# Kernel optimization log

Measured on AMD Instinct MI355X. Metric: run time of the kernel, lower is better.

Reference implementation:

```python
import jax, jax.numpy as jnp
import numpy as np

K = 3        # prediction_steps
SKIP = 1     # skip_step (forward default)
NEG = 64     # opt.negative_samples
EPS = 1e-11  # ExpNLLLoss epsilon


def setup_inputs() -> dict:
    key = jax.random.key(0)
    ks = jax.random.split(key, 8)
    B, C, H, W = 64, 256, 14, 14
    z = jax.random.normal(ks[0], (B, C, H, W), jnp.float32)
    c = jax.random.normal(ks[1], (B, C, H, W), jnp.float32)
    Wk = jax.random.normal(ks[2], (K, C, C), jnp.float32) / np.sqrt(C).astype(np.float32)
    inp = {"z": z, "c": c, "Wk": Wk}
    for k in range(1, K + 1):
        Hp = H - (k + SKIP)
        rows = Hp * W * B
        inp[f"neg_idx_k{k}"] = jax.random.randint(ks[2 + k], (rows * NEG,), 0, rows, dtype=jnp.int32)
    return inp


def _loss_k(z, c, Wk, neg_idx, k):
    # z, c: [B,C,H,W]; Wk: [Co,Ci] (1x1 conv); neg_idx: [(H-k-SKIP)*W*B*NEG]
    B, C, H, W = z.shape
    Hp = H - (k + SKIP)
    zt = z[:, :, k + SKIP:, :]                            # [B,Ci,Hp,W]
    ztwk = jnp.einsum('oc,bchw->hwbo', Wk, zt)            # [Hp,W,B,Co] (1x1 conv + permute(2,3,0,1))
    flat = ztwk.reshape(Hp * W * B, -1)
    shuf = flat[neg_idx].reshape(Hp, W, B, NEG, -1)       # gathered negatives [Hp,W,B,N,Co]
    ctx = jnp.transpose(c[:, :, :Hp, :], (2, 3, 0, 1))    # context c[:,:,:-(k+SKIP),:] -> [Hp,W,B,Co]
    main = jnp.einsum('hwbc,hwbc->hwb', ctx, ztwk)[..., None]   # [Hp,W,B,1]
    negs = jnp.einsum('hwbc,hwbnc->hwbn', ctx, shuf)            # [Hp,W,B,N]
    log_fk = jnp.concatenate([main, negs], axis=-1)             # [Hp,W,B,1+N]
    log_fk = jnp.transpose(log_fk, (2, 3, 0, 1))                # [B,1+N,Hp,W]
    probs = jax.nn.softmax(log_fk, axis=1)
    # ExpNLLLoss, target class 0, reduction='mean'
    return -jnp.mean(jnp.log(probs[:, 0] + EPS))


def reference(z, c, Wk, neg_idx_k1, neg_idx_k2, neg_idx_k3):
    idxs = [neg_idx_k1, neg_idx_k2, neg_idx_k3]
    total = 0.0
    for k in range(1, K + 1):
        total = total + _loss_k(z, c, Wk[k - 1], idxs[k - 1], k)
    return total / K
```

## Files before the change

### kernel.cpp

```cpp
#include <hip/hip_runtime.h>
#include <math.h>


typedef short bf16x8 __attribute__((ext_vector_type(8)));
typedef float f32x4 __attribute__((ext_vector_type(4)));

static __device__ __forceinline__ unsigned short f2bf(float f) {
    union { float f; unsigned int u; } x; x.f = f;
    unsigned int r = x.u + 0x7fffu + ((x.u >> 16) & 1u);
    return (unsigned short)(r >> 16);
}

static __device__ __forceinline__ unsigned char f2e4m3(float f) {
    union { float f; unsigned int u; } x; x.f = f;
    unsigned int s = (x.u >> 24) & 0x80u;
    float af = fabsf(f);
    if (af > 448.f) af = 448.f;
    x.f = af;
    unsigned int u = x.u;
    int e = (int)(u >> 23) - 127;
    unsigned int out;
    if (af == 0.f) {
        out = 0u;
    } else if (e < -6) {
        int mq = (int)rintf(af * 512.f);
        out = (mq >= 8) ? 0x08u : (unsigned int)mq;
    } else {
        unsigned int r = u + 0x7FFFFu + ((u >> 20) & 1u);
        int e2 = (int)(r >> 23) - 127;
        if (e2 > 8) out = 0x7Eu;
        else out = (unsigned int)(((e2 + 7) << 3) | ((r >> 20) & 7u));
    }
    return (unsigned char)(s | out);
}

static __device__ __forceinline__ void gload_lds4(const void* g, void* l) {
    __builtin_amdgcn_global_load_lds(
        (const __attribute__((address_space(1))) void*)g,
        (__attribute__((address_space(3))) void*)l, 4, 0, 0);
}

__global__ __launch_bounds__(256)
void prep_kernel(const float* __restrict__ z, const float* __restrict__ c,
                 const float* __restrict__ Wk,
                 unsigned short* __restrict__ zt, unsigned char* __restrict__ ct8,
                 unsigned short* __restrict__ wkb, float* __restrict__ out) {
    __shared__ float tile[16][201];
    const int tid = threadIdx.x;
    int x = blockIdx.x;
    if (x < 768) {
        int i = x * 256 + tid;
        wkb[i] = f2bf(Wk[i]);
        if (x == 0 && tid == 0) out[0] = 0.f;
        return;
    }
    const bool isz = x < 1792;
    const int local = isz ? (x - 768) : (x - 1792);
    const float* src = isz ? z : c;
    const int b  = local & 63;
    const int c0 = (local >> 6) << 4;
    for (int i = tid; i < 16 * 196; i += 256) {
        int cc = i / 196;
        int hw = i - cc * 196;
        tile[cc][hw] = src[(size_t)((b << 8) + c0 + cc) * 196 + hw];
    }
    __syncthreads();
    if (isz) {
        for (int i = tid; i < 196 * 16; i += 256) {
            int hw = i >> 4, cc = i & 15;
            zt[(size_t)((hw << 6) + b) * 256 + c0 + cc] = f2bf(tile[cc][hw]);
        }
    } else {
        for (int i = tid; i < 196 * 16; i += 256) {
            int hw = i >> 4, cc = i & 15;
            ct8[(size_t)((hw << 6) + b) * 256 + c0 + cc] = f2e4m3(tile[cc][hw]);
        }
    }
}

#define PSTR 544
__global__ __launch_bounds__(256)
void proj_mfma_kernel(const unsigned short* __restrict__ zt,
                      const unsigned short* __restrict__ wkb,
                      unsigned char* __restrict__ ztwk) {
    __shared__ __align__(16) unsigned char smem[(64 + 32) * PSTR];
    unsigned char* smA = smem;
    unsigned char* smB = smem + 64 * PSTR;

    int x = blockIdx.x;
    int k, hw;
    if (x < 168)      { k = 0; hw = x; }
    else if (x < 322) { k = 1; hw = x - 168; }
    else              { k = 2; hw = x - 322; }
    const int o0 = blockIdx.y << 5;
    const int row0  = hw << 6;
    const int zrow0 = row0 + (((k + 2) * 14) << 6);
    unsigned char* zo = ztwk + (size_t)k * 10752 * 256;

    const int tid = threadIdx.x;
    const unsigned char* zsrc = (const unsigned char*)(zt + (size_t)zrow0 * 256);
    const unsigned char* bsrc = (const unsigned char*)(wkb + ((size_t)k << 16) + o0 * 256);

    #pragma unroll
    for (int i = 0; i < 8; ++i) {
        int sb = ((i << 8) + tid) << 4;
        int r = sb >> 9, off = sb & 511;
        *(int4*)(smA + r * PSTR + off) = *(const int4*)(zsrc + sb);
    }
    #pragma unroll
    for (int i = 0; i < 4; ++i) {
        int sb = ((i << 8) + tid) << 4;
        int r = sb >> 9, off = sb & 511;
        *(int4*)(smB + r * PSTR + off) = *(const int4*)(bsrc + sb);
    }
    __syncthreads();

    const int wv = tid >> 6, lane = tid & 63;
    const int m = lane & 15, kq = lane >> 4;
    f32x4 acc[2] = {};
    const unsigned short* aP  = (const unsigned short*)(smA + (size_t)((wv << 4) + m) * PSTR) + (kq << 3);
    const unsigned short* bP0 = (const unsigned short*)(smB + (size_t)m * PSTR) + (kq << 3);
    const unsigned short* bP1 = (const unsigned short*)(smB + (size_t)(16 + m) * PSTR) + (kq << 3);
    #pragma unroll
    for (int kk = 0; kk < 256; kk += 32) {
        bf16x8 af = *(const bf16x8*)(aP  + kk);
        bf16x8 b0 = *(const bf16x8*)(bP0 + kk);
        bf16x8 b1 = *(const bf16x8*)(bP1 + kk);
        acc[0] = __builtin_amdgcn_mfma_f32_16x16x32_bf16(af, b0, acc[0], 0, 0, 0);
        acc[1] = __builtin_amdgcn_mfma_f32_16x16x32_bf16(af, b1, acc[1], 0, 0, 0);
    }
    __syncthreads();
    unsigned char* cs = smA;
    #pragma unroll
    for (int nt = 0; nt < 2; ++nt)
        #pragma unroll
        for (int r = 0; r < 4; ++r)
            cs[(size_t)((wv << 4) + (kq << 2) + r) * 40 + (nt << 4) + m] =
                f2e4m3(acc[nt][r]);
    __syncthreads();
    {
        int r = tid >> 2, off = (tid & 3) << 3;
        unsigned long long v = *(const unsigned long long*)(cs + (size_t)r * 40 + off);
        *(unsigned long long*)(zo + (size_t)(row0 + r) * 256 + o0 + off) = v;
    }
}

#define ROWB 272
#define TPB 16
__global__ __launch_bounds__(128, 2)
void loss_mfma_kernel(const unsigned char* __restrict__ ct8,
                      const unsigned char* __restrict__ ztwk8,
                      const int* __restrict__ n0, const int* __restrict__ n1,
                      const int* __restrict__ n2, float* __restrict__ rowloss) {
    __shared__ __align__(16) unsigned char slab[2][65 * ROWB];
    __shared__ __align__(16) unsigned char ctx_s[2][256];
    const int tid = threadIdx.x;
    const int wv = tid >> 6, lane = tid & 63;
    const int m = lane & 15, kq = lane >> 4;

    const int task0 = blockIdx.x * TPB;
    int k; const int* nb; int segbase;
    if (task0 < 10752)      { k = 0; nb = n0; segbase = 0; }
    else if (task0 < 20608) { k = 1; nb = n1; segbase = 10752; }
    else                    { k = 2; nb = n2; segbase = 20608; }
    const int row0 = task0 - segbase;
    const unsigned char* flat8 = ztwk8 + (size_t)k * 10752 * 256;
    const float wkf = (k == 0) ? (1.f / (3.f * 10752.f))
                    : (k == 1) ? (1.f / (3.f * 9856.f))
                               : (1.f / (3.f * 8960.f));

    int myidx_next = 0;
    if (wv == 1) {
        int idx0 = nb[((size_t)row0 << 6) + lane];
        gload_lds4(flat8 + (size_t)row0 * 256 + (lane << 2), &slab[0][0]);
        gload_lds4(ct8 + (size_t)row0 * 256 + (lane << 2), &ctx_s[0][0]);
        #pragma unroll
        for (int j = 1; j <= 64; ++j) {
            int idx = __builtin_amdgcn_readlane(idx0, j - 1);
            gload_lds4(flat8 + (size_t)idx * 256 + (lane << 2), &slab[0][j * ROWB]);
        }
        myidx_next = nb[((size_t)(row0 + 1) << 6) + lane];
    }
    __syncthreads();

    int soff[5];
    #pragma unroll
    for (int mt = 0; mt < 5; ++mt) {
        int slot = (mt << 4) + m;
        if (slot > 64) slot = 64;
        soff[mt] = slot * ROWB + (kq << 3);
    }

    for (int t = 0; t < TPB; ++t) {
        const int buf = t & 1;
        if (wv == 1) {
            if (t + 1 < TPB) {
                const int rn = row0 + t + 1;
                const int nbuf = buf ^ 1;
                gload_lds4(flat8 + (size_t)rn * 256 + (lane << 2), &slab[nbuf][0]);
                gload_lds4(ct8 + (size_t)rn * 256 + (lane << 2), &ctx_s[nbuf][0]);
                #pragma unroll
                for (int j = 1; j <= 64; ++j) {
                    int idx = __builtin_amdgcn_readlane(myidx_next, j - 1);
                    gload_lds4(flat8 + (size_t)idx * 256 + (lane << 2),
                               &slab[nbuf][j * ROWB]);
                }
                if (t + 2 < TPB)
                    myidx_next = nb[((size_t)(row0 + t + 2) << 6) + lane];
            }
        } else {
            f32x4 acc[5] = {};
            const unsigned char* sl = &slab[buf][0];
            const unsigned char* cp = &ctx_s[buf][kq << 3];
            #pragma unroll
            for (int kk = 0; kk < 8; ++kk) {
                long long bfrag = *(const long long*)(cp + (kk << 5));
                #pragma unroll
                for (int mt = 0; mt < 5; ++mt) {
                    long long af = *(const long long*)(sl + soff[mt] + (kk << 5));
                    acc[mt] = __builtin_amdgcn_mfma_f32_16x16x32_fp8_fp8(
                        af, bfrag, acc[mt], 0, 0, 0);
                }
            }
            float m_l = -1e30f;
            #pragma unroll
            for (int mt = 0; mt < 4; ++mt)
                #pragma unroll
                for (int r = 0; r < 4; ++r) m_l = fmaxf(m_l, acc[mt][r]);
            if (kq == 0) m_l = fmaxf(m_l, acc[4][0]);
            m_l = fmaxf(m_l, __shfl_xor(m_l, 16));
            m_l = fmaxf(m_l, __shfl_xor(m_l, 32));
            float s_l = 0.f;
            #pragma unroll
            for (int mt = 0; mt < 4; ++mt)
                #pragma unroll
                for (int r = 0; r < 4; ++r) s_l += __expf(acc[mt][r] - m_l);
            if (kq == 0) s_l += __expf(acc[4][0] - m_l);
            s_l += __shfl_xor(s_l, 16);
            s_l += __shfl_xor(s_l, 32);
            if (lane == 0) {
                float p0 = __expf(acc[0][0] - m_l) / s_l;
                rowloss[segbase + row0 + t] = -logf(p0 + 1e-11f) * wkf;
            }
        }
        __syncthreads();
    }
}

__global__ __launch_bounds__(256)
void reduce_kernel(const float* __restrict__ rl, float* __restrict__ out) {
    float s = 0.f;
    const int stride = gridDim.x * blockDim.x;
    for (int i = blockIdx.x * blockDim.x + threadIdx.x; i < 29568; i += stride)
        s += rl[i];
    #pragma unroll
    for (int off = 32; off >= 1; off >>= 1) s += __shfl_xor(s, off);
    if ((threadIdx.x & 63) == 0) atomicAdd(out, s);
}

extern "C" void kernel_launch(void* const* d_in, const int* in_sizes, int n_in,
                              void* d_out, int out_size, void* d_ws, size_t ws_size,
                              hipStream_t stream) {
    const float* z  = (const float*)d_in[0];
    const float* c  = (const float*)d_in[1];
    const float* Wk = (const float*)d_in[2];
    const int* negs[3] = {(const int*)d_in[3], (const int*)d_in[4], (const int*)d_in[5]};
    float* out = (float*)d_out;

    char* p = (char*)d_ws;
    unsigned short* zt      = (unsigned short*)p;   p += (size_t)196 * 64 * 256 * 2;
    unsigned short* wkb     = (unsigned short*)p;   p += (size_t)3 * 65536 * 2;
    unsigned char*  ct8     = (unsigned char*)p;    p += (size_t)196 * 64 * 256;
    unsigned char*  ztwk8   = (unsigned char*)p;    p += (size_t)3 * 10752 * 256;
    float*          rowloss = (float*)p;

    prep_kernel<<<2816, 256, 0, stream>>>(z, c, Wk, zt, ct8, wkb, out);
    proj_mfma_kernel<<<dim3(462, 8), 256, 0, stream>>>(zt, wkb, ztwk8);
    loss_mfma_kernel<<<1848, 128, 0, stream>>>(ct8, ztwk8, negs[0], negs[1],
                                               negs[2], rowloss);
    reduce_kernel<<<32, 256, 0, stream>>>(rowloss, out);
}
```

Measured before the change: 167.8 us.

## Replace producer/consumer wave split with independent per-wave load-then-compute rows

```diff
diff --git a/kernel.cpp b/kernel.cpp
--- a/kernel.cpp
+++ b/kernel.cpp
@@ -146,43 +146,31 @@
 }
 
 #define ROWB 272
-#define TPB 16
-__global__ __launch_bounds__(128, 2)
+#define SLABSZ (65 * ROWB + 272)
+__global__ __launch_bounds__(128)
 void loss_mfma_kernel(const unsigned char* __restrict__ ct8,
                       const unsigned char* __restrict__ ztwk8,
                       const int* __restrict__ n0, const int* __restrict__ n1,
                       const int* __restrict__ n2, float* __restrict__ rowloss) {
-    __shared__ __align__(16) unsigned char slab[2][65 * ROWB];
-    __shared__ __align__(16) unsigned char ctx_s[2][256];
+    __shared__ __align__(16) unsigned char lds[2][SLABSZ];
     const int tid = threadIdx.x;
     const int wv = tid >> 6, lane = tid & 63;
     const int m = lane & 15, kq = lane >> 4;
-
-    const int task0 = blockIdx.x * TPB;
+    unsigned char* sl  = lds[wv];
+    unsigned char* ctx = sl + 65 * ROWB;
+
+    const int W = (blockIdx.x << 1) + wv;
+    const int base = W << 3;
     int k; const int* nb; int segbase;
-    if (task0 < 10752)      { k = 0; nb = n0; segbase = 0; }
-    else if (task0 < 20608) { k = 1; nb = n1; segbase = 10752; }
-    else                    { k = 2; nb = n2; segbase = 20608; }
-    const int row0 = task0 - segbase;
+    if (base < 10752)      { k = 0; nb = n0; segbase = 0; }
+    else if (base < 20608) { k = 1; nb = n1; segbase = 10752; }
+    else                   { k = 2; nb = n2; segbase = 20608; }
+    const int row0 = base - segbase;
     const unsigned char* flat8 = ztwk8 + (size_t)k * 10752 * 256;
     const float wkf = (k == 0) ? (1.f / (3.f * 10752.f))
                     : (k == 1) ? (1.f / (3.f * 9856.f))
                                : (1.f / (3.f * 8960.f));
 
-    int myidx_next = 0;
-    if (wv == 1) {
-        int idx0 = nb[((size_t)row0 << 6) + lane];
-        gload_lds4(flat8 + (size_t)row0 * 256 + (lane << 2), &slab[0][0]);
-        gload_lds4(ct8 + (size_t)row0 * 256 + (lane << 2), &ctx_s[0][0]);
-        #pragma unroll
-        for (int j = 1; j <= 64; ++j) {
-            int idx = __builtin_amdgcn_readlane(idx0, j - 1);
-            gload_lds4(flat8 + (size_t)idx * 256 + (lane << 2), &slab[0][j * ROWB]);
-        }
-        myidx_next = nb[((size_t)(row0 + 1) << 6) + lane];
-    }
-    __syncthreads();
-
     int soff[5];
     #pragma unroll
     for (int mt = 0; mt < 5; ++mt) {
@@ -191,59 +179,55 @@
         soff[mt] = slot * ROWB + (kq << 3);
     }
 
-    for (int t = 0; t < TPB; ++t) {
-        const int buf = t & 1;
-        if (wv == 1) {
-            if (t + 1 < TPB) {
-                const int rn = row0 + t + 1;
-                const int nbuf = buf ^ 1;
-                gload_lds4(flat8 + (size_t)rn * 256 + (lane << 2), &slab[nbuf][0]);
-                gload_lds4(ct8 + (size_t)rn * 256 + (lane << 2), &ctx_s[nbuf][0]);
-                #pragma unroll
-                for (int j = 1; j <= 64; ++j) {
-                    int idx = __builtin_amdgcn_readlane(myidx_next, j - 1);
-                    gload_lds4(flat8 + (size_t)idx * 256 + (lane << 2),
-                               &slab[nbuf][j * ROWB]);
-                }
-                if (t + 2 < TPB)
-                    myidx_next = nb[((size_t)(row0 + t + 2) << 6) + lane];
+    int myidx = nb[((size_t)row0 << 6) + lane];
+
+    for (int t = 0; t < 8; ++t) {
+        const int row = row0 + t;
+        asm volatile("s_waitcnt lgkmcnt(0)" ::: "memory");
+        gload_lds4(flat8 + (size_t)row * 256 + (lane << 2), sl);
+        gload_lds4(ct8 + (size_t)row * 256 + (lane << 2), ctx);
+        #pragma unroll
+        for (int j = 1; j <= 64; ++j) {
+            int idx = __builtin_amdgcn_readlane(myidx, j - 1);
+            gload_lds4(flat8 + (size_t)idx * 256 + (lane << 2), sl + j * ROWB);
+        }
+        asm volatile("s_waitcnt vmcnt(0)" ::: "memory");
+        if (t + 1 < 8)
+            myidx = nb[((size_t)(row + 1) << 6) + lane];
+
+        f32x4 acc[5] = {};
+        const unsigned char* cp = ctx + (kq << 3);
+        #pragma unroll
+        for (int kk = 0; kk < 8; ++kk) {
+            long long bfrag = *(const long long*)(cp + (kk << 5));
+            #pragma unroll
+            for (int mt = 0; mt < 5; ++mt) {
+                long long af = *(const long long*)(sl + soff[mt] + (kk << 5));
+                acc[mt] = __builtin_amdgcn_mfma_f32_16x16x32_fp8_fp8(
+                    af, bfrag, acc[mt], 0, 0, 0);
             }
-        } else {
-            f32x4 acc[5] = {};
-            const unsigned char* sl = &slab[buf][0];
-            const unsigned char* cp = &ctx_s[buf][kq << 3];
+        }
+
+        float m_l = -1e30f;
+        #pragma unroll
+        for (int mt = 0; mt < 4; ++mt)
             #pragma unroll
-            for (int kk = 0; kk < 8; ++kk) {
-                long long bfrag = *(const long long*)(cp + (kk << 5));
-                #pragma unroll
-                for (int mt = 0; mt < 5; ++mt) {
-                    long long af = *(const long long*)(sl + soff[mt] + (kk << 5));
-                    acc[mt] = __builtin_amdgcn_mfma_f32_16x16x32_fp8_fp8(
-                        af, bfrag, acc[mt], 0, 0, 0);
-                }
-            }
-            float m_l = -1e30f;
+            for (int r = 0; r < 4; ++r) m_l = fmaxf(m_l, acc[mt][r]);
+        if (kq == 0) m_l = fmaxf(m_l, acc[4][0]);
+        m_l = fmaxf(m_l, __shfl_xor(m_l, 16));
+        m_l = fmaxf(m_l, __shfl_xor(m_l, 32));
+        float s_l = 0.f;
+        #pragma unroll
+        for (int mt = 0; mt < 4; ++mt)
             #pragma unroll
-            for (int mt = 0; mt < 4; ++mt)
-                #pragma unroll
-                for (int r = 0; r < 4; ++r) m_l = fmaxf(m_l, acc[mt][r]);
-            if (kq == 0) m_l = fmaxf(m_l, acc[4][0]);
-            m_l = fmaxf(m_l, __shfl_xor(m_l, 16));
-            m_l = fmaxf(m_l, __shfl_xor(m_l, 32));
-            float s_l = 0.f;
-            #pragma unroll
-            for (int mt = 0; mt < 4; ++mt)
-                #pragma unroll
-                for (int r = 0; r < 4; ++r) s_l += __expf(acc[mt][r] - m_l);
-            if (kq == 0) s_l += __expf(acc[4][0] - m_l);
-            s_l += __shfl_xor(s_l, 16);
-            s_l += __shfl_xor(s_l, 32);
-            if (lane == 0) {
-                float p0 = __expf(acc[0][0] - m_l) / s_l;
-                rowloss[segbase + row0 + t] = -logf(p0 + 1e-11f) * wkf;
-            }
-        }
-        __syncthreads();
+            for (int r = 0; r < 4; ++r) s_l += __expf(acc[mt][r] - m_l);
+        if (kq == 0) s_l += __expf(acc[4][0] - m_l);
+        s_l += __shfl_xor(s_l, 16);
+        s_l += __shfl_xor(s_l, 32);
+        if (lane == 0) {
+            float p0 = __expf(acc[0][0] - m_l) / s_l;
+            rowloss[base + t] = -logf(p0 + 1e-11f) * wkf;
+        }
     }
 }
 
```

Result: no change. 169.0 us (+0.7%).
